# Kernel optimization log

Hardware: AMD Instinct MI355X
Metric: run time of the kernel (lower is better)

The kernel has to match this reference:

```python
import jax, jax.numpy as jnp
import numpy as np

N_NODES = 100000
N_EDGES = 1600000
IN_DIM, H1, H2, OUT_DIM = 256, 128, 64, 32
EPS = 1e-12  # tf.nn.l2_normalize epsilon


def setup_inputs() -> dict:
    key = jax.random.key(0)
    ks = jax.random.split(key, 8)
    features = jax.random.normal(ks[0], (N_NODES, IN_DIM), dtype=jnp.float32)
    edge_vals = jax.random.uniform(ks[1], (N_EDGES,), dtype=jnp.float32)
    # Glorot-uniform weights as in glorot()
    def glorot(k, shape):
        r = np.sqrt(6.0 / (shape[0] + shape[1]))
        return jax.random.uniform(k, shape, minval=-r, maxval=r, dtype=jnp.float32)
    W0 = glorot(ks[2], (IN_DIM, H1))
    W1 = glorot(ks[3], (H1, H2))
    W2 = glorot(ks[4], (H2, OUT_DIM))
    edge_row = jax.random.randint(ks[5], (N_EDGES,), 0, N_NODES, dtype=jnp.int32)
    edge_col = jax.random.randint(ks[6], (N_EDGES,), 0, N_NODES, dtype=jnp.int32)
    return {"features": features, "edge_vals": edge_vals, "W0": W0, "W1": W1,
            "W2": W2, "edge_row": edge_row, "edge_col": edge_col}


def reference(features, edge_vals, W0, W1, W2, edge_row, edge_col):
    # tf.nn.l2_normalize(features, axis=1)
    sq = jnp.sum(features * features, axis=1, keepdims=True)
    x = features * jax.lax.rsqrt(jnp.maximum(sq, EPS))

    def spmm(h):  # support @ h, support sparse in COO form
        msgs = edge_vals[:, None] * h[edge_col]           # [E, d]
        return jax.ops.segment_sum(msgs, edge_row, num_segments=N_NODES)

    h = jax.nn.relu(spmm(x @ W0))      # layer 1
    h = jax.nn.relu(spmm(h @ W1))      # layer 2
    out = spmm(h @ W2)                 # layer 3, identity act
    return out
```

## Files before the change

### kernel.cpp

```cpp
#include <hip/hip_runtime.h>


constexpr int IN_DIM = 256, HD1 = 128, HD2 = 64, OUT_DIM = 32;
constexpr int SCAN_CHUNK = 2048;

typedef __bf16 bf16x8 __attribute__((ext_vector_type(8)));
typedef float f32x4 __attribute__((ext_vector_type(4)));

__device__ inline ushort f32_to_bf16(float x) {
    unsigned u = __float_as_uint(x);
    unsigned r = (u + 0x7fff + ((u >> 16) & 1)) >> 16;
    return (ushort)r;
}

__device__ inline void unpack_bf16x2(unsigned u, float& lo, float& hi) {
    lo = __uint_as_float(u << 16);
    hi = __uint_as_float(u & 0xffff0000u);
}

__global__ __launch_bounds__(256) void l2norm_kernel(const float* __restrict__ in,
                                                     ushort* __restrict__ out, int M) {
    int wave = threadIdx.x >> 6;
    int lane = threadIdx.x & 63;
    int row = blockIdx.x * 4 + wave;
    if (row >= M) return;
    const float4 v = *reinterpret_cast<const float4*>(&in[(size_t)row * IN_DIM + lane * 4]);
    float s = v.x * v.x + v.y * v.y + v.z * v.z + v.w * v.w;
    #pragma unroll
    for (int off = 32; off; off >>= 1) s += __shfl_xor(s, off, 64);
    float scale = 1.0f / sqrtf(fmaxf(s, 1e-12f));
    uint2 pk;
    pk.x = (unsigned)f32_to_bf16(v.x * scale) | ((unsigned)f32_to_bf16(v.y * scale) << 16);
    pk.y = (unsigned)f32_to_bf16(v.z * scale) | ((unsigned)f32_to_bf16(v.w * scale) << 16);
    *reinterpret_cast<uint2*>(&out[(size_t)row * IN_DIM + lane * 4]) = pk;
}

__global__ __launch_bounds__(256) void wt_kernel(const float* __restrict__ W,
                                                 ushort* __restrict__ WT, int K, int N) {
    int idx = blockIdx.x * 256 + threadIdx.x;
    if (idx < K * N) {
        int k = idx / N, n = idx % N;
        WT[(size_t)n * K + k] = f32_to_bf16(W[idx]);
    }
}

__global__ __launch_bounds__(256) void hist_kernel(const int* __restrict__ row,
                                                   int* __restrict__ counts, int E) {
    int e = blockIdx.x * blockDim.x + threadIdx.x;
    if (e < E) atomicAdd(&counts[row[e]], 1);
}

__global__ __launch_bounds__(256) void scan_partial(const int* __restrict__ counts,
                                                    int* __restrict__ bsum, int n) {
    __shared__ int sm[256];
    const int tid = threadIdx.x;
    const int base = blockIdx.x * SCAN_CHUNK + tid * 8;
    int s = 0;
    #pragma unroll
    for (int i = 0; i < 8; ++i) {
        int idx = base + i;
        if (idx < n) s += counts[idx];
    }
    sm[tid] = s;
    __syncthreads();
    #pragma unroll
    for (int off = 128; off; off >>= 1) {
        if (tid < off) sm[tid] += sm[tid + off];
        __syncthreads();
    }
    if (tid == 0) bsum[blockIdx.x] = sm[0];
}

__global__ __launch_bounds__(256) void scan_blocksums(const int* __restrict__ bsum,
                                                      int* __restrict__ boff, int nblk) {
    __shared__ int sm[256];
    const int tid = threadIdx.x;
    int v = (tid < nblk) ? bsum[tid] : 0;
    sm[tid] = v;
    __syncthreads();
    #pragma unroll
    for (int off = 1; off < 256; off <<= 1) {
        int t = (tid >= off) ? sm[tid - off] : 0;
        __syncthreads();
        sm[tid] += t;
        __syncthreads();
    }
    if (tid < nblk) boff[tid] = sm[tid] - v;
    if (tid == 255) boff[nblk] = sm[255];
}

__global__ __launch_bounds__(256) void scan_final(const int* __restrict__ counts,
                                                  const int* __restrict__ boff,
                                                  int* __restrict__ row_ptr, int n, int nblk) {
    __shared__ int sm[256];
    const int tid = threadIdx.x;
    const int base = blockIdx.x * SCAN_CHUNK + tid * 8;
    int c[8];
    int s = 0;
    #pragma unroll
    for (int i = 0; i < 8; ++i) {
        int idx = base + i;
        c[i] = (idx < n) ? counts[idx] : 0;
        s += c[i];
    }
    sm[tid] = s;
    __syncthreads();
    #pragma unroll
    for (int off = 1; off < 256; off <<= 1) {
        int t = (tid >= off) ? sm[tid - off] : 0;
        __syncthreads();
        sm[tid] += t;
        __syncthreads();
    }
    int run = boff[blockIdx.x] + sm[tid] - s;
    #pragma unroll
    for (int i = 0; i < 8; ++i) {
        int idx = base + i;
        if (idx < n) row_ptr[idx] = run;
        run += c[i];
    }
    if (blockIdx.x == 0 && tid == 0) row_ptr[n] = boff[nblk];
}

__global__ __launch_bounds__(256) void scatter_kernel(const int* __restrict__ row,
                                                      const int* __restrict__ col,
                                                      const float* __restrict__ val,
                                                      const int* __restrict__ row_ptr,
                                                      int* __restrict__ row_cur,
                                                      int2* __restrict__ pairs, int E) {
    int e = blockIdx.x * blockDim.x + threadIdx.x;
    if (e < E) {
        int r = row[e];
        int pos = row_ptr[r] + atomicAdd(&row_cur[r], 1);
        pairs[pos] = make_int2(col[e], __float_as_int(val[e]));
    }
}

template <int BN, int WM, int WN>
__global__ __launch_bounds__(256) void gemm_bf16_mfma(
    const ushort* __restrict__ A, const ushort* __restrict__ BT,
    ushort* __restrict__ C, int K) {
    constexpr int BM = 128, BK = 64;
    constexpr int FM = BM / WM / 16;
    constexpr int FN = BN / WN / 16;
    __shared__ ushort As[BM * BK];
    __shared__ ushort Bs[BN * BK];
    const int tid = threadIdx.x;
    const int lane = tid & 63;
    const int wid = tid >> 6;
    const int wm = wid / WN;
    const int wn = wid % WN;
    const int row0 = blockIdx.x * BM;
    const size_t strideB = (size_t)K * 2;

    f32x4 acc[FM][FN] = {};

    const int lkb = ((lane >> 4) << 4) ^ ((lane & 7) << 4);
    const int laneOff = (lane & 15) * 128 + lkb;

    for (int k0 = 0; k0 < K; k0 += BK) {
        {
            constexpr int per_wave = BM * 128 / 4;
            const char* gbase = (const char*)(A + (size_t)row0 * K);
            #pragma unroll
            for (int i = 0; i < per_wave / 1024; ++i) {
                int o = wid * per_wave + i * 1024 + lane * 16;
                int row = o >> 7;
                int kb = (o & 127) ^ ((row & 7) << 4);
                const char* src = gbase + (size_t)row * strideB + (size_t)k0 * 2 + kb;
                ushort* dst = As + (wid * per_wave + i * 1024) / 2;
                __builtin_amdgcn_global_load_lds(
                    (const __attribute__((address_space(1))) unsigned int*)src,
                    (__attribute__((address_space(3))) unsigned int*)dst, 16, 0, 0);
            }
        }
        {
            constexpr int per_wave = BN * 128 / 4;
            const char* gbase = (const char*)BT;
            #pragma unroll
            for (int i = 0; i < per_wave / 1024; ++i) {
                int o = wid * per_wave + i * 1024 + lane * 16;
                int row = o >> 7;
                int kb = (o & 127) ^ ((row & 7) << 4);
                const char* src = gbase + (size_t)row * strideB + (size_t)k0 * 2 + kb;
                ushort* dst = Bs + (wid * per_wave + i * 1024) / 2;
                __builtin_amdgcn_global_load_lds(
                    (const __attribute__((address_space(1))) unsigned int*)src,
                    (__attribute__((address_space(3))) unsigned int*)dst, 16, 0, 0);
            }
        }
        __syncthreads();

        #pragma unroll
        for (int w = 0; w < BK / 32; ++w) {
            bf16x8 af[FM], bfr[FN];
            #pragma unroll
            for (int mi = 0; mi < FM; ++mi) {
                int byte = wm * FM * 2048 + mi * 2048 + (laneOff ^ (w << 6));
                af[mi] = *(const bf16x8*)((const char*)As + byte);
            }
            #pragma unroll
            for (int ni = 0; ni < FN; ++ni) {
                int byte = wn * FN * 2048 + ni * 2048 + (laneOff ^ (w << 6));
                bfr[ni] = *(const bf16x8*)((const char*)Bs + byte);
            }
            #pragma unroll
            for (int mi = 0; mi < FM; ++mi)
                #pragma unroll
                for (int ni = 0; ni < FN; ++ni)
                    acc[mi][ni] = __builtin_amdgcn_mfma_f32_16x16x32_bf16(
                        af[mi], bfr[ni], acc[mi][ni], 0, 0, 0);
        }
        __syncthreads();
    }

    #pragma unroll
    for (int mi = 0; mi < FM; ++mi) {
        #pragma unroll
        for (int ni = 0; ni < FN; ++ni) {
            int rbase = row0 + wm * FM * 16 + mi * 16 + ((lane >> 4) << 2);
            int col = wn * FN * 16 + ni * 16 + (lane & 15);
            #pragma unroll
            for (int r = 0; r < 4; ++r)
                C[(size_t)(rbase + r) * BN + col] = f32_to_bf16(acc[mi][ni][r]);
        }
    }
}

template <int D, bool RELU, bool OUTF32>
__global__ __launch_bounds__(256) void spmm_bf16(const int* __restrict__ row_ptr,
                                                 const int2* __restrict__ pairs,
                                                 const ushort* __restrict__ H,
                                                 void* __restrict__ outp, int M) {
    constexpr int TPR = D / 8;
    const int rpb = 256 / TPR;
    const int lg = threadIdx.x % TPR;
    const int rloc = threadIdx.x / TPR;
    int r = blockIdx.x * rpb + rloc;
    if (r >= M) return;
    const int jb = row_ptr[r], je = row_ptr[r + 1];
    float acc[8] = {};
    int j = jb;
    for (; j + 1 < je; j += 2) {
        int2 p0 = pairs[j];
        int2 p1 = pairs[j + 1];
        uint4 u0 = *reinterpret_cast<const uint4*>(&H[(size_t)p0.x * D + lg * 8]);
        uint4 u1 = *reinterpret_cast<const uint4*>(&H[(size_t)p1.x * D + lg * 8]);
        float v0 = __int_as_float(p0.y), v1 = __int_as_float(p1.y);
        float f[8];
        unpack_bf16x2(u0.x, f[0], f[1]); unpack_bf16x2(u0.y, f[2], f[3]);
        unpack_bf16x2(u0.z, f[4], f[5]); unpack_bf16x2(u0.w, f[6], f[7]);
        #pragma unroll
        for (int i = 0; i < 8; ++i) acc[i] = fmaf(v0, f[i], acc[i]);
        unpack_bf16x2(u1.x, f[0], f[1]); unpack_bf16x2(u1.y, f[2], f[3]);
        unpack_bf16x2(u1.z, f[4], f[5]); unpack_bf16x2(u1.w, f[6], f[7]);
        #pragma unroll
        for (int i = 0; i < 8; ++i) acc[i] = fmaf(v1, f[i], acc[i]);
    }
    if (j < je) {
        int2 p0 = pairs[j];
        uint4 u0 = *reinterpret_cast<const uint4*>(&H[(size_t)p0.x * D + lg * 8]);
        float v0 = __int_as_float(p0.y);
        float f[8];
        unpack_bf16x2(u0.x, f[0], f[1]); unpack_bf16x2(u0.y, f[2], f[3]);
        unpack_bf16x2(u0.z, f[4], f[5]); unpack_bf16x2(u0.w, f[6], f[7]);
        #pragma unroll
        for (int i = 0; i < 8; ++i) acc[i] = fmaf(v0, f[i], acc[i]);
    }
    if (RELU) {
        #pragma unroll
        for (int i = 0; i < 8; ++i) acc[i] = fmaxf(acc[i], 0.f);
    }
    if (OUTF32) {
        float* dst = (float*)outp + (size_t)r * D + lg * 8;
        *reinterpret_cast<float4*>(dst) = *reinterpret_cast<const float4*>(&acc[0]);
        *reinterpret_cast<float4*>(dst + 4) = *reinterpret_cast<const float4*>(&acc[4]);
    } else {
        uint4 pk;
        pk.x = (unsigned)f32_to_bf16(acc[0]) | ((unsigned)f32_to_bf16(acc[1]) << 16);
        pk.y = (unsigned)f32_to_bf16(acc[2]) | ((unsigned)f32_to_bf16(acc[3]) << 16);
        pk.z = (unsigned)f32_to_bf16(acc[4]) | ((unsigned)f32_to_bf16(acc[5]) << 16);
        pk.w = (unsigned)f32_to_bf16(acc[6]) | ((unsigned)f32_to_bf16(acc[7]) << 16);
        *reinterpret_cast<uint4*>((ushort*)outp + (size_t)r * D + lg * 8) = pk;
    }
}

extern "C" void kernel_launch(void* const* d_in, const int* in_sizes, int n_in,
                              void* d_out, int out_size, void* d_ws, size_t ws_size,
                              hipStream_t stream) {
    const float* features  = (const float*)d_in[0];
    const float* edge_vals = (const float*)d_in[1];
    const float* W0        = (const float*)d_in[2];
    const float* W1        = (const float*)d_in[3];
    const float* W2        = (const float*)d_in[4];
    const int*   edge_row  = (const int*)d_in[5];
    const int*   edge_col  = (const int*)d_in[6];
    const int M = in_sizes[0] / IN_DIM;
    const int E = in_sizes[1];
    const int Mp = ((M + 127) / 128) * 128;

    char* ws = (char*)d_ws;
    size_t o = 0;
    auto alloc = [&](size_t bytes) {
        size_t r = o;
        o += (bytes + 1023) & ~(size_t)1023;
        return r;
    };
    ushort* XH    = (ushort*)(ws + alloc((size_t)Mp * IN_DIM * 2));
    ushort* T     = (ushort*)(ws + alloc((size_t)Mp * HD1 * 2));
    size_t counts_off = alloc((size_t)M * 4);
    int*   counts = (int*)(ws + counts_off);
    int*   rowcur = (int*)(ws + alloc((size_t)M * 4));
    size_t rowptr_off = alloc((size_t)(M + 1) * 4);
    int*   rowptr = (int*)(ws + rowptr_off);
    int2*  pairs  = (int2*)(ws + alloc((size_t)E * 8));
    const int nblk_scan = (M + SCAN_CHUNK - 1) / SCAN_CHUNK;
    int*   bsum   = (int*)(ws + alloc((size_t)256 * 4));
    int*   boff   = (int*)(ws + alloc((size_t)257 * 4));
    ushort* W0T   = (ushort*)(ws + alloc((size_t)HD1 * IN_DIM * 2));
    ushort* W1T   = (ushort*)(ws + alloc((size_t)HD2 * HD1 * 2));
    ushort* W2T   = (ushort*)(ws + alloc((size_t)OUT_DIM * HD2 * 2));
    float* out = (float*)d_out;
    (void)ws_size; (void)n_in; (void)out_size;

    hipMemsetAsync(ws + counts_off, 0, rowptr_off - counts_off, stream);

    hist_kernel<<<(E + 255) / 256, 256, 0, stream>>>(edge_row, counts, E);
    scan_partial<<<nblk_scan, 256, 0, stream>>>(counts, bsum, M);
    scan_blocksums<<<1, 256, 0, stream>>>(bsum, boff, nblk_scan);
    scan_final<<<nblk_scan, 256, 0, stream>>>(counts, boff, rowptr, M, nblk_scan);
    scatter_kernel<<<(E + 255) / 256, 256, 0, stream>>>(edge_row, edge_col, edge_vals,
                                                        rowptr, rowcur, pairs, E);

    wt_kernel<<<(IN_DIM * HD1 + 255) / 256, 256, 0, stream>>>(W0, W0T, IN_DIM, HD1);
    wt_kernel<<<(HD1 * HD2 + 255) / 256, 256, 0, stream>>>(W1, W1T, HD1, HD2);
    wt_kernel<<<(HD2 * OUT_DIM + 255) / 256, 256, 0, stream>>>(W2, W2T, HD2, OUT_DIM);

    l2norm_kernel<<<(M + 3) / 4, 256, 0, stream>>>(features, XH, M);

    const int gblk = Mp / 128;

    gemm_bf16_mfma<128, 2, 2><<<gblk, 256, 0, stream>>>(XH, W0T, T, IN_DIM);
    spmm_bf16<128, true, false><<<(M + 15) / 16, 256, 0, stream>>>(rowptr, pairs, T, XH, M);

    gemm_bf16_mfma<64, 2, 2><<<gblk, 256, 0, stream>>>(XH, W1T, T, HD1);
    spmm_bf16<64, true, false><<<(M + 31) / 32, 256, 0, stream>>>(rowptr, pairs, T, XH, M);

    gemm_bf16_mfma<32, 4, 1><<<gblk, 256, 0, stream>>>(XH, W2T, T, HD2);
    spmm_bf16<32, false, true><<<(M + 63) / 64, 256, 0, stream>>>(rowptr, pairs, T, out, M);
}
```

Baseline: 497.0 us.

## Replace global-atomic COO-to-CSR build with two-pass bucketed LDS counting sort

Measured after the change: 413.3 us. 1.2x faster.

```diff
diff --git a/kernel.cpp b/kernel.cpp
--- a/kernel.cpp
+++ b/kernel.cpp
@@ -2,7 +2,7 @@
 
 
 constexpr int IN_DIM = 256, HD1 = 128, HD2 = 64, OUT_DIM = 32;
-constexpr int SCAN_CHUNK = 2048;
+constexpr int P1B = 256;
 
 typedef __bf16 bf16x8 __attribute__((ext_vector_type(8)));
 typedef float f32x4 __attribute__((ext_vector_type(4)));
@@ -44,38 +44,28 @@
     }
 }
 
-__global__ __launch_bounds__(256) void hist_kernel(const int* __restrict__ row,
-                                                   int* __restrict__ counts, int E) {
-    int e = blockIdx.x * blockDim.x + threadIdx.x;
-    if (e < E) atomicAdd(&counts[row[e]], 1);
-}
-
-__global__ __launch_bounds__(256) void scan_partial(const int* __restrict__ counts,
-                                                    int* __restrict__ bsum, int n) {
+
+__global__ __launch_bounds__(256) void bucket_count(const int* __restrict__ row,
+                                                    int* __restrict__ blockcnt,
+                                                    int E, int nbuk, int epb) {
+    __shared__ int cnt[512];
+    for (int i = threadIdx.x; i < nbuk; i += 256) cnt[i] = 0;
+    __syncthreads();
+    const int base = blockIdx.x * epb;
+    const int end = min(E, base + epb);
+    for (int e = base + threadIdx.x; e < end; e += 256)
+        atomicAdd(&cnt[row[e] >> 8], 1);
+    __syncthreads();
+    for (int i = threadIdx.x; i < nbuk; i += 256)
+        blockcnt[i * P1B + blockIdx.x] = cnt[i];
+}
+
+__global__ __launch_bounds__(256) void scan_bucket_blocks(const int* __restrict__ blockcnt,
+                                                          int* __restrict__ blockoff,
+                                                          int* __restrict__ bucketcnt) {
     __shared__ int sm[256];
-    const int tid = threadIdx.x;
-    const int base = blockIdx.x * SCAN_CHUNK + tid * 8;
-    int s = 0;
-    #pragma unroll
-    for (int i = 0; i < 8; ++i) {
-        int idx = base + i;
-        if (idx < n) s += counts[idx];
-    }
-    sm[tid] = s;
-    __syncthreads();
-    #pragma unroll
-    for (int off = 128; off; off >>= 1) {
-        if (tid < off) sm[tid] += sm[tid + off];
-        __syncthreads();
-    }
-    if (tid == 0) bsum[blockIdx.x] = sm[0];
-}
-
-__global__ __launch_bounds__(256) void scan_blocksums(const int* __restrict__ bsum,
-                                                      int* __restrict__ boff, int nblk) {
-    __shared__ int sm[256];
-    const int tid = threadIdx.x;
-    int v = (tid < nblk) ? bsum[tid] : 0;
+    const int b = blockIdx.x, tid = threadIdx.x;
+    const int v = blockcnt[b * P1B + tid];
     sm[tid] = v;
     __syncthreads();
     #pragma unroll
@@ -85,54 +75,85 @@
         sm[tid] += t;
         __syncthreads();
     }
-    if (tid < nblk) boff[tid] = sm[tid] - v;
-    if (tid == 255) boff[nblk] = sm[255];
-}
-
-__global__ __launch_bounds__(256) void scan_final(const int* __restrict__ counts,
-                                                  const int* __restrict__ boff,
-                                                  int* __restrict__ row_ptr, int n, int nblk) {
-    __shared__ int sm[256];
+    blockoff[b * P1B + tid] = sm[tid] - v;
+    if (tid == 255) bucketcnt[b] = sm[255];
+}
+
+__global__ __launch_bounds__(512) void scan_bucket_base(const int* __restrict__ bucketcnt,
+                                                        int* __restrict__ bucket_base, int nbuk) {
+    __shared__ int sm[512];
     const int tid = threadIdx.x;
-    const int base = blockIdx.x * SCAN_CHUNK + tid * 8;
-    int c[8];
-    int s = 0;
-    #pragma unroll
-    for (int i = 0; i < 8; ++i) {
-        int idx = base + i;
-        c[i] = (idx < n) ? counts[idx] : 0;
-        s += c[i];
-    }
-    sm[tid] = s;
+    const int v = (tid < nbuk) ? bucketcnt[tid] : 0;
+    sm[tid] = v;
+    __syncthreads();
+    #pragma unroll
+    for (int off = 1; off < 512; off <<= 1) {
+        int t = (tid >= off) ? sm[tid - off] : 0;
+        __syncthreads();
+        sm[tid] += t;
+        __syncthreads();
+    }
+    if (tid < nbuk) bucket_base[tid] = sm[tid] - v;
+    if (tid == 511) bucket_base[nbuk] = sm[511];
+}
+
+__global__ __launch_bounds__(256) void bucket_place(const int* __restrict__ row,
+                                                    const int* __restrict__ col,
+                                                    const float* __restrict__ val,
+                                                    const int* __restrict__ blockoff,
+                                                    const int* __restrict__ bucket_base,
+                                                    int2* __restrict__ ebuf,
+                                                    int E, int nbuk, int epb) {
+    __shared__ int pos[512];
+    for (int i = threadIdx.x; i < nbuk; i += 256)
+        pos[i] = bucket_base[i] + blockoff[i * P1B + blockIdx.x];
+    __syncthreads();
+    const int base = blockIdx.x * epb;
+    const int end = min(E, base + epb);
+    for (int e = base + threadIdx.x; e < end; e += 256) {
+        int r = row[e];
+        int b = r >> 8;
+        int p = atomicAdd(&pos[b], 1);
+        ebuf[p] = make_int2(col[e] | ((r & 255) << 17), __float_as_int(val[e]));
+    }
+}
+
+__global__ __launch_bounds__(256) void bucket_csr(const int2* __restrict__ ebuf,
+                                                  const int* __restrict__ bucket_base,
+                                                  int2* __restrict__ pairs,
+                                                  int* __restrict__ row_ptr,
+                                                  int M, int nbuk) {
+    __shared__ int cnt[256];
+    __shared__ int pos[256];
+    const int b = blockIdx.x, tid = threadIdx.x;
+    const int start = bucket_base[b], end = bucket_base[b + 1];
+    cnt[tid] = 0;
+    __syncthreads();
+    for (int j = start + tid; j < end; j += 256)
+        atomicAdd(&cnt[(ebuf[j].x >> 17) & 255], 1);
+    __syncthreads();
+    const int v = cnt[tid];
+    pos[tid] = v;
     __syncthreads();
     #pragma unroll
     for (int off = 1; off < 256; off <<= 1) {
-        int t = (tid >= off) ? sm[tid - off] : 0;
-        __syncthreads();
-        sm[tid] += t;
-        __syncthreads();
-    }
-    int run = boff[blockIdx.x] + sm[tid] - s;
-    #pragma unroll
-    for (int i = 0; i < 8; ++i) {
-        int idx = base + i;
-        if (idx < n) row_ptr[idx] = run;
-        run += c[i];
-    }
-    if (blockIdx.x == 0 && tid == 0) row_ptr[n] = boff[nblk];
-}
-
-__global__ __launch_bounds__(256) void scatter_kernel(const int* __restrict__ row,
-                                                      const int* __restrict__ col,
-                                                      const float* __restrict__ val,
-                                                      const int* __restrict__ row_ptr,
-                                                      int* __restrict__ row_cur,
-                                                      int2* __restrict__ pairs, int E) {
-    int e = blockIdx.x * blockDim.x + threadIdx.x;
-    if (e < E) {
-        int r = row[e];
-        int pos = row_ptr[r] + atomicAdd(&row_cur[r], 1);
-        pairs[pos] = make_int2(col[e], __float_as_int(val[e]));
+        int t = (tid >= off) ? pos[tid - off] : 0;
+        __syncthreads();
+        pos[tid] += t;
+        __syncthreads();
+    }
+    const int excl = pos[tid] - v;
+    const int rg = b * 256 + tid;
+    if (rg < M) row_ptr[rg] = start + excl;
+    if (rg == M) row_ptr[M] = start + excl;
+    __syncthreads();
+    cnt[tid] = excl;
+    __syncthreads();
+    for (int j = start + tid; j < end; j += 256) {
+        int2 e = ebuf[j];
+        int rlow = (e.x >> 17) & 255;
+        int p = atomicAdd(&cnt[rlow], 1);
+        pairs[start + p] = make_int2(e.x & 0x1FFFF, e.y);
     }
 }
 
@@ -298,6 +319,8 @@
     const int M = in_sizes[0] / IN_DIM;
     const int E = in_sizes[1];
     const int Mp = ((M + 127) / 128) * 128;
+    const int nbuk = (M + 255) >> 8;
+    const int epb = (E + P1B - 1) / P1B;
 
     char* ws = (char*)d_ws;
     size_t o = 0;
@@ -306,31 +329,27 @@
         o += (bytes + 1023) & ~(size_t)1023;
         return r;
     };
-    ushort* XH    = (ushort*)(ws + alloc((size_t)Mp * IN_DIM * 2));
-    ushort* T     = (ushort*)(ws + alloc((size_t)Mp * HD1 * 2));
-    size_t counts_off = alloc((size_t)M * 4);
-    int*   counts = (int*)(ws + counts_off);
-    int*   rowcur = (int*)(ws + alloc((size_t)M * 4));
-    size_t rowptr_off = alloc((size_t)(M + 1) * 4);
-    int*   rowptr = (int*)(ws + rowptr_off);
-    int2*  pairs  = (int2*)(ws + alloc((size_t)E * 8));
-    const int nblk_scan = (M + SCAN_CHUNK - 1) / SCAN_CHUNK;
-    int*   bsum   = (int*)(ws + alloc((size_t)256 * 4));
-    int*   boff   = (int*)(ws + alloc((size_t)257 * 4));
-    ushort* W0T   = (ushort*)(ws + alloc((size_t)HD1 * IN_DIM * 2));
-    ushort* W1T   = (ushort*)(ws + alloc((size_t)HD2 * HD1 * 2));
-    ushort* W2T   = (ushort*)(ws + alloc((size_t)OUT_DIM * HD2 * 2));
+    ushort* XH      = (ushort*)(ws + alloc((size_t)Mp * IN_DIM * 2));
+    ushort* T       = (ushort*)(ws + alloc((size_t)Mp * HD1 * 2));
+    int*   rowptr   = (int*)(ws + alloc((size_t)(M + 2) * 4));
+    int2*  pairs    = (int2*)(ws + alloc((size_t)E * 8));
+    int2*  ebuf     = (int2*)(ws + alloc((size_t)E * 8));
+    int*   blockcnt = (int*)(ws + alloc((size_t)512 * P1B * 4));
+    int*   blockoff = (int*)(ws + alloc((size_t)512 * P1B * 4));
+    int*   bucketcnt= (int*)(ws + alloc((size_t)512 * 4));
+    int*   bucketbase=(int*)(ws + alloc((size_t)513 * 4));
+    ushort* W0T     = (ushort*)(ws + alloc((size_t)HD1 * IN_DIM * 2));
+    ushort* W1T     = (ushort*)(ws + alloc((size_t)HD2 * HD1 * 2));
+    ushort* W2T     = (ushort*)(ws + alloc((size_t)OUT_DIM * HD2 * 2));
     float* out = (float*)d_out;
     (void)ws_size; (void)n_in; (void)out_size;
 
-    hipMemsetAsync(ws + counts_off, 0, rowptr_off - counts_off, stream);
-
-    hist_kernel<<<(E + 255) / 256, 256, 0, stream>>>(edge_row, counts, E);
-    scan_partial<<<nblk_scan, 256, 0, stream>>>(counts, bsum, M);
-    scan_blocksums<<<1, 256, 0, stream>>>(bsum, boff, nblk_scan);
-    scan_final<<<nblk_scan, 256, 0, stream>>>(counts, boff, rowptr, M, nblk_scan);
-    scatter_kernel<<<(E + 255) / 256, 256, 0, stream>>>(edge_row, edge_col, edge_vals,
-                                                        rowptr, rowcur, pairs, E);
+    bucket_count<<<P1B, 256, 0, stream>>>(edge_row, blockcnt, E, nbuk, epb);
+    scan_bucket_blocks<<<nbuk, 256, 0, stream>>>(blockcnt, blockoff, bucketcnt);
+    scan_bucket_base<<<1, 512, 0, stream>>>(bucketcnt, bucketbase, nbuk);
+    bucket_place<<<P1B, 256, 0, stream>>>(edge_row, edge_col, edge_vals,
+                                          blockoff, bucketbase, ebuf, E, nbuk, epb);
+    bucket_csr<<<nbuk, 256, 0, stream>>>(ebuf, bucketbase, pairs, rowptr, M, nbuk);
 
     wt_kernel<<<(IN_DIM * HD1 + 255) / 256, 256, 0, stream>>>(W0, W0T, IN_DIM, HD1);
     wt_kernel<<<(HD1 * HD2 + 255) / 256, 256, 0, stream>>>(W1, W1T, HD1, HD2);
```
